# Optimization experiments

Hardware: AMD Instinct MI355X
Metric: run time of the kernel (lower is better)

The kernel has to match this reference:

```python
import jax, jax.numpy as jnp
import numpy as np

B, N, C, H = 16, 4096, 256, 4
D = C // H


def setup_inputs() -> dict:
    key = jax.random.key(0)
    ks = jax.random.split(key, 16)
    s = 0.02
    inp = {
        "x": jax.random.normal(ks[0], (B, N, C), jnp.float32),
        "encoding": jax.random.normal(ks[1], (2, B, 1, N, D), jnp.float32),
        "Wqkv_w": jax.random.normal(ks[2], (3 * C, C), jnp.float32) * s,
        "Wqkv_b": jnp.zeros((3 * C,), jnp.float32),
        "tssa_qkv_w": jax.random.normal(ks[3], (C, C), jnp.float32) * s,
        "tssa_qkv_b": jnp.zeros((C,), jnp.float32),
        "temp": jnp.ones((H, 1), jnp.float32),
        "tssa_out_w": jax.random.normal(ks[4], (C, C), jnp.float32) * s,
        "tssa_out_b": jnp.zeros((C,), jnp.float32),
        "out_proj_w": jax.random.normal(ks[5], (C, C), jnp.float32) * s,
        "out_proj_b": jnp.zeros((C,), jnp.float32),
        "ffn1_w": jax.random.normal(ks[6], (2 * C, 2 * C), jnp.float32) * s,
        "ffn1_b": jnp.zeros((2 * C,), jnp.float32),
        "ln_g": jnp.ones((2 * C,), jnp.float32),
        "ln_b": jnp.zeros((2 * C,), jnp.float32),
        "ffn2_w": jax.random.normal(ks[7], (C, 2 * C), jnp.float32) * s,
        "ffn2_b": jnp.zeros((C,), jnp.float32),
    }
    return inp


def _rotate_half(t):
    # (..., d) -> pairwise rotate: (x1, x2) -> (-x2, x1)
    t2 = t.reshape(t.shape[:-1] + (-1, 2))
    x1, x2 = t2[..., 0], t2[..., 1]
    return jnp.stack((-x2, x1), axis=-1).reshape(t.shape)


def reference(x, encoding, Wqkv_w, Wqkv_b, tssa_qkv_w, tssa_qkv_b, temp,
              tssa_out_w, tssa_out_b, out_proj_w, out_proj_b,
              ffn1_w, ffn1_b, ln_g, ln_b, ffn2_w, ffn2_b):
    b, n, c = x.shape
    h, d = H, D
    # QKV projection, layout (h, d, 3) on last dim as in unflatten(-1,(h,-1,3))
    qkv = (x @ Wqkv_w.T + Wqkv_b).reshape(b, n, h, d, 3).transpose(0, 2, 1, 3, 4)  # b h n d 3
    q, k, v = qkv[..., 0], qkv[..., 1], qkv[..., 2]
    rope = lambda t: t * encoding[0] + _rotate_half(t) * encoding[1]
    q = rope(q)
    k = rope(k)
    flat = lambda t: t.transpose(0, 2, 1, 3).reshape(b, n, c)  # b h n d -> b n (h d)
    w_input = (flat(q) + flat(k) + flat(v)) / 3.0
    # TSSA attention
    w = (w_input @ tssa_qkv_w.T + tssa_qkv_b).reshape(b, n, h, d).transpose(0, 2, 1, 3)  # b h n d
    norm = jnp.sqrt(jnp.sum(w * w, axis=2, keepdims=True))  # L2 over sequence axis N
    w_normed = w / jnp.maximum(norm, 1e-12)
    sum_ws = jnp.sum(w_normed * w_normed, axis=-1)  # b h n
    Pi = jax.nn.softmax(sum_ws * temp[None, :, :], axis=1)  # softmax over heads
    Pi_norm = Pi / (jnp.sum(Pi, axis=-1, keepdims=True) + 1e-8)
    dots = jnp.einsum('bhn,bhnd->bh', Pi_norm, w * w)  # (b,h,1,d) summed over d
    attn = 1.0 / (1.0 + dots)  # b h
    out = -(w * Pi[..., None]) * attn[:, :, None, None]  # b h n d
    out = out.transpose(0, 2, 1, 3).reshape(b, n, c)
    context = out @ tssa_out_w.T + tssa_out_b
    message = context @ out_proj_w.T + out_proj_b
    # residual FFN
    cat = jnp.concatenate([x, message], axis=-1)  # b n 2c
    h1 = cat @ ffn1_w.T + ffn1_b
    mu = jnp.mean(h1, axis=-1, keepdims=True)
    var = jnp.mean((h1 - mu) ** 2, axis=-1, keepdims=True)
    ln = (h1 - mu) / jnp.sqrt(var + 1e-5) * ln_g + ln_b
    g = jax.nn.gelu(ln, approximate=False)
    return x + (g @ ffn2_w.T + ffn2_b)
```

## Files before the change

kernel.cpp:

```cpp
#include <hip/hip_runtime.h>
#include <math.h>

#define Bc 16
#define Nc 4096

typedef __attribute__((ext_vector_type(8))) short short8;
typedef __attribute__((ext_vector_type(4))) float floatx4;

__device__ __forceinline__ unsigned short f2bf(float f) {
    union { float f; unsigned int u; } v; v.f = f;
    unsigned int u = v.u;
    return (unsigned short)((u + 0x7fffu + ((u >> 16) & 1u)) >> 16);
}
__device__ __forceinline__ float bf2f(unsigned short u) {
    union { unsigned int u; float f; } v; v.u = ((unsigned int)u) << 16;
    return v.f;
}

__device__ __forceinline__ float gelu_f(float x) {
    const float z = x * 0.70710678118654752f;
    const float az = fabsf(z);
    const float t = 1.f / (1.f + 0.3275911f * az);
    const float poly = t * (0.254829592f + t * (-0.284496736f +
                       t * (1.421413741f + t * (-1.453152027f + t * 1.061405429f))));
    const float e = __expf(-z * z);
    const float er = copysignf(1.f - poly * e, z);
    return 0.5f * x * (1.f + er);
}

__device__ __forceinline__ void gll16(const unsigned short* g, unsigned short* l) {
    __builtin_amdgcn_global_load_lds(
        (const __attribute__((address_space(1))) void*)g,
        (__attribute__((address_space(3))) void*)l,
        16, 0, 0);
}

template <int EPI, typename TOUT>
__global__ __launch_bounds__(512) void gemm_bf(
    const unsigned short* __restrict__ A0, int lda0,
    const unsigned short* __restrict__ A1, int lda1, int K0,
    const unsigned short* __restrict__ W,
    const float* __restrict__ bias,
    const unsigned short* __restrict__ resid_bf,
    const float* __restrict__ Pi,
    const float* __restrict__ Sb,
    const float* __restrict__ Tb,
    float* __restrict__ norm2,
    float* __restrict__ rowstats,
    const float* __restrict__ enc,
    const float* __restrict__ lng,
    const float* __restrict__ lnb,
    TOUT* __restrict__ C, int N, int K)
{
    __shared__ alignas(16) unsigned short As[128 * 64];
    __shared__ alignas(16) unsigned short Bs[256 * 64];

    const int t = threadIdx.x;
    const int bn = blockIdx.x, bm = blockIdx.y;
    const int lane = t & 63, wave = t >> 6;
    const int wm = wave >> 2, wn = wave & 3;
    const int quad = lane >> 4, l16 = lane & 15;
    const int rt = t >> 3, st = t & 7;

    float mean0 = 0.f, rstd0 = 0.f, mean1 = 0.f, rstd1 = 0.f;
    if constexpr (EPI == 3) {
        const size_t g0 = (size_t)bm * 128 + rt;
        const float2 s0 = *(const float2*)(rowstats + g0 * 2);
        const float2 s1 = *(const float2*)(rowstats + (g0 + 64) * 2);
        mean0 = s0.x * (1.f / 512.f);
        rstd0 = rsqrtf(s0.y * (1.f / 512.f) - mean0 * mean0 + 1e-5f);
        mean1 = s1.x * (1.f / 512.f);
        rstd1 = rsqrtf(s1.y * (1.f / 512.f) - mean1 * mean1 + 1e-5f);
    }

    floatx4 acc[4][4];
    #pragma unroll
    for (int i = 0; i < 4; ++i)
        #pragma unroll
        for (int j = 0; j < 4; ++j)
            acc[i][j] = (floatx4){0.f, 0.f, 0.f, 0.f};

    for (int k0 = 0; k0 < K; k0 += 64) {
        #pragma unroll
        for (int hh = 0; hh < 2; ++hh) {
            const int row = hh * 64 + rt;
            const int col = k0 + (st ^ (row & 7)) * 8;
            unsigned short* ldsa = As + row * 64 + st * 8;
            const size_t grow = (size_t)bm * 128 + row;
            if constexpr (EPI == 2) {
                const int b = (int)(grow >> 12);
                const int hd = col >> 6;
                const float Sv = Sb[b * 4 + hd], Tv = Tb[b * 4 + hd];
                const float at = 1.f / (1.f + Tv / (Sv + 1e-8f));
                const float sc = -Pi[grow * 4 + hd] * at;
                const short8 a = *(const short8*)(A0 + grow * (size_t)lda0 + col);
                short8 o;
                #pragma unroll
                for (int j = 0; j < 8; ++j) o[j] = (short)f2bf(bf2f((unsigned short)a[j]) * sc);
                *(short8*)ldsa = o;
            } else if constexpr (EPI == 3) {
                const float mean = hh ? mean1 : mean0;
                const float rstd = hh ? rstd1 : rstd0;
                const short8 a = *(const short8*)(A0 + grow * (size_t)lda0 + col);
                const float4 ga = *(const float4*)(lng + col);
                const float4 gb = *(const float4*)(lng + col + 4);
                const float4 ba = *(const float4*)(lnb + col);
                const float4 bb = *(const float4*)(lnb + col + 4);
                const float vg[8] = {ga.x, ga.y, ga.z, ga.w, gb.x, gb.y, gb.z, gb.w};
                const float vb[8] = {ba.x, ba.y, ba.z, ba.w, bb.x, bb.y, bb.z, bb.w};
                short8 o;
                #pragma unroll
                for (int jj = 0; jj < 8; ++jj) {
                    const float ln = (bf2f((unsigned short)a[jj]) - mean) * rstd * vg[jj] + vb[jj];
                    o[jj] = (short)f2bf(gelu_f(ln));
                }
                *(short8*)ldsa = o;
            } else {
                const unsigned short* src = (col < K0)
                    ? (A0 + grow * (size_t)lda0 + col)
                    : (A1 + grow * (size_t)lda1 + (col - K0));
                gll16(src, ldsa);
            }
        }
        #pragma unroll
        for (int hh = 0; hh < 4; ++hh) {
            const int row = hh * 64 + rt;
            const int col = k0 + (st ^ (row & 7)) * 8;
            gll16(W + ((size_t)bn * 256 + row) * (size_t)K + col, Bs + row * 64 + st * 8);
        }
        __syncthreads();
        #pragma unroll
        for (int kk = 0; kk < 2; ++kk) {
            short8 af[4], wf[4];
            #pragma unroll
            for (int i = 0; i < 4; ++i) {
                const int ra = wm * 64 + i * 16 + l16;
                af[i] = *(const short8*)(As + ra * 64 + ((quad + kk * 4) ^ (ra & 7)) * 8);
                const int rw = wn * 64 + i * 16 + l16;
                wf[i] = *(const short8*)(Bs + rw * 64 + ((quad + kk * 4) ^ (rw & 7)) * 8);
            }
            #pragma unroll
            for (int mi = 0; mi < 4; ++mi)
                #pragma unroll
                for (int ni = 0; ni < 4; ++ni)
                    acc[mi][ni] = __builtin_amdgcn_mfma_f32_16x16x32_bf16(
                        wf[ni], af[mi], acc[mi][ni], 0, 0, 0);
        }
        __syncthreads();
    }

    float rs[4], rq[4];
    if constexpr (EPI == 4) {
        #pragma unroll
        for (int m = 0; m < 4; ++m) { rs[m] = 0.f; rq[m] = 0.f; }
    }

    #pragma unroll
    for (int mi = 0; mi < 4; ++mi) {
        const size_t row = (size_t)bm * 128 + wm * 64 + mi * 16 + l16;
        #pragma unroll
        for (int ni = 0; ni < 4; ++ni) {
            const int cb = bn * 256 + wn * 64 + ni * 16 + quad * 4;
            const float4 b4 = *(const float4*)(bias + cb);
            if constexpr (EPI == 5) {
                const float s0 = acc[mi][ni][0] + b4.x;
                const float v0 = acc[mi][ni][1] + b4.y;
                const float s1 = acc[mi][ni][2] + b4.z;
                const float v1 = acc[mi][ni][3] + b4.w;
                const int j = cb >> 1;
                const int d = j & 63;
                const float2 e0 = *(const float2*)(enc + row * 64 + d);
                const float2 e1 = *(const float2*)(enc + 4194304 + row * 64 + d);
                const float r0 = s0 * e0.x - s1 * e1.x;
                const float r1 = s1 * e0.y + s0 * e1.y;
                ushort2 o;
                o.x = f2bf((r0 + v0) * (1.f / 3.f));
                o.y = f2bf((r1 + v1) * (1.f / 3.f));
                *(ushort2*)((unsigned short*)C + row * (size_t)N + j) = o;
            } else {
                float v[4] = {acc[mi][ni][0] + b4.x, acc[mi][ni][1] + b4.y,
                              acc[mi][ni][2] + b4.z, acc[mi][ni][3] + b4.w};
                if constexpr (EPI == 3) {
                    const ushort4 xr = *(const ushort4*)(resid_bf + row * (size_t)N + cb);
                    v[0] += bf2f(xr.x); v[1] += bf2f(xr.y);
                    v[2] += bf2f(xr.z); v[3] += bf2f(xr.w);
                }
                if constexpr (EPI == 4) {
                    #pragma unroll
                    for (int rg = 0; rg < 4; ++rg) { rs[mi] += v[rg]; rq[mi] += v[rg] * v[rg]; }
                }
                if constexpr (EPI == 1) {
                    float cs[4];
                    #pragma unroll
                    for (int rg = 0; rg < 4; ++rg) cs[rg] = v[rg] * v[rg];
                    #pragma unroll
                    for (int rg = 0; rg < 4; ++rg) {
                        float s = cs[rg];
                        s += __shfl_xor(s, 1, 64);
                        s += __shfl_xor(s, 2, 64);
                        s += __shfl_xor(s, 4, 64);
                        s += __shfl_xor(s, 8, 64);
                        if (l16 == 0) atomicAdd(&norm2[(bm >> 5) * 256 + cb + rg], s);
                    }
                }
                if constexpr (__is_same(TOUT, float)) {
                    float4 o; o.x = v[0]; o.y = v[1]; o.z = v[2]; o.w = v[3];
                    *(float4*)(C + row * (size_t)N + cb) = o;
                } else {
                    ushort4 o;
                    o.x = f2bf(v[0]); o.y = f2bf(v[1]); o.z = f2bf(v[2]); o.w = f2bf(v[3]);
                    *(ushort4*)(C + row * (size_t)N + cb) = o;
                }
            }
        }
    }
    if constexpr (EPI == 4) {
        #pragma unroll
        for (int mi = 0; mi < 4; ++mi) {
            float s = rs[mi], q = rq[mi];
            s += __shfl_xor(s, 16, 64); s += __shfl_xor(s, 32, 64);
            q += __shfl_xor(q, 16, 64); q += __shfl_xor(q, 32, 64);
            if (quad == 0) {
                const size_t row = (size_t)bm * 128 + wm * 64 + mi * 16 + l16;
                atomicAdd(&rowstats[row * 2], s);
                atomicAdd(&rowstats[row * 2 + 1], q);
            }
        }
    }
}

__device__ __forceinline__ void conv8(const float* src, unsigned short* dst, int i) {
    const float4 f0 = *(const float4*)(src + (size_t)i * 8);
    const float4 f1 = *(const float4*)(src + (size_t)i * 8 + 4);
    short8 sv;
    sv[0] = (short)f2bf(f0.x); sv[1] = (short)f2bf(f0.y);
    sv[2] = (short)f2bf(f0.z); sv[3] = (short)f2bf(f0.w);
    sv[4] = (short)f2bf(f1.x); sv[5] = (short)f2bf(f1.y);
    sv[6] = (short)f2bf(f1.z); sv[7] = (short)f2bf(f1.w);
    *(short8*)(dst + (size_t)i * 8) = sv;
}

__global__ __launch_bounds__(256) void prep_all(
    const float* __restrict__ x, const float* __restrict__ Wqkv,
    const float* __restrict__ bqkv, const float* __restrict__ tssa_w,
    const float* __restrict__ op_w, const float* __restrict__ to_w,
    const float* __restrict__ to_b, const float* __restrict__ op_b,
    const float* __restrict__ f1w, const float* __restrict__ f2w,
    unsigned short* __restrict__ x_bf, unsigned short* __restrict__ Wsv,
    float* __restrict__ bsv, unsigned short* __restrict__ tssa_bf,
    unsigned short* __restrict__ Wf, float* __restrict__ bfb,
    unsigned short* __restrict__ ffn1_bf, unsigned short* __restrict__ ffn2_bf,
    float* __restrict__ zbase, float* __restrict__ rowstats)
{
    const int blk = blockIdx.x, tt = threadIdx.x;
    if (blk < 8192) {
        conv8(x, x_bf, blk * 256 + tt);
    } else if (blk < 8704) {
        const int r = blk - 8192, c = tt;
        const int j = r >> 1;
        const int h = j >> 6, dd = j & 63;
        const int base = h * 192 + dd * 3;
        if (!(r & 1)) {
            Wsv[r * 256 + c] = f2bf(Wqkv[(base + 0) * 256 + c] + Wqkv[(base + 1) * 256 + c]);
            if (c == 0) bsv[r] = bqkv[base] + bqkv[base + 1];
        } else {
            Wsv[r * 256 + c] = f2bf(Wqkv[(base + 2) * 256 + c]);
            if (c == 0) bsv[r] = bqkv[base + 2];
        }
    } else if (blk < 8960) {
        const int i = blk - 8704;
        float s = 0.f;
        for (int k = 0; k < 256; ++k) s += op_w[i * 256 + k] * to_w[k * 256 + tt];
        Wf[i * 256 + tt] = f2bf(s);
    } else if (blk == 8960) {
        float s = op_b[tt];
        for (int k = 0; k < 256; ++k) s += op_w[tt * 256 + k] * to_b[k];
        bfb[tt] = s;
    } else if (blk < 8993) {
        conv8(tssa_w, tssa_bf, (blk - 8961) * 256 + tt);
    } else if (blk < 9121) {
        conv8(f1w, ffn1_bf, (blk - 8993) * 256 + tt);
    } else if (blk < 9185) {
        conv8(f2w, ffn2_bf, (blk - 9121) * 256 + tt);
    } else {
        const int i = (blk - 9185) * 256 + tt;
        if (i < 4288) zbase[i] = 0.f;
        else if (i < 135360) rowstats[i - 4288] = 0.f;
    }
}

__global__ __launch_bounds__(256) void pi_kernel(const unsigned short* __restrict__ w,
                                                 const float* __restrict__ norm2,
                                                 const float* __restrict__ temp,
                                                 float* __restrict__ Pi,
                                                 float* __restrict__ S,
                                                 float* __restrict__ T) {
    const int t = threadIdx.x;
    const int i = t & 15;
    const int lr = t >> 4;
    const size_t r = (size_t)blockIdx.x * 16 + lr;
    const int b = (int)(r >> 12);
    const unsigned short* wrow = w + r * 256;
    const float* n2row = norm2 + b * 256;
    float raw[4], nrm[4];
    #pragma unroll
    for (int h = 0; h < 4; ++h) {
        const ushort4 wv = *(const ushort4*)(wrow + h * 64 + i * 4);
        const float w0 = bf2f(wv.x), w1 = bf2f(wv.y), w2 = bf2f(wv.z), w3 = bf2f(wv.w);
        const float4 n2 = *(const float4*)(n2row + h * 64 + i * 4);
        const float s0 = w0 * w0, s1 = w1 * w1, s2 = w2 * w2, s3 = w3 * w3;
        raw[h] = s0 + s1 + s2 + s3;
        nrm[h] = s0 / fmaxf(n2.x, 1e-24f) + s1 / fmaxf(n2.y, 1e-24f)
               + s2 / fmaxf(n2.z, 1e-24f) + s3 / fmaxf(n2.w, 1e-24f);
    }
    #pragma unroll
    for (int off = 1; off < 16; off <<= 1) {
        #pragma unroll
        for (int h = 0; h < 4; ++h) {
            raw[h] += __shfl_xor(raw[h], off, 64);
            nrm[h] += __shfl_xor(nrm[h], off, 64);
        }
    }
    float sw[4], m = -1e30f;
    #pragma unroll
    for (int h = 0; h < 4; ++h) { sw[h] = nrm[h] * temp[h]; m = fmaxf(m, sw[h]); }
    float e[4], Z = 0.f;
    #pragma unroll
    for (int h = 0; h < 4; ++h) { e[h] = expf(sw[h] - m); Z += e[h]; }
    const float invZ = 1.f / Z;
    float pi[4];
    #pragma unroll
    for (int h = 0; h < 4; ++h) pi[h] = e[h] * invZ;
    if (i < 4) Pi[r * 4 + i] = pi[i];

    __shared__ float sS[16][4], sT[16][4];
    if (i == 0) {
        #pragma unroll
        for (int h = 0; h < 4; ++h) { sS[lr][h] = pi[h]; sT[lr][h] = pi[h] * raw[h]; }
    }
    __syncthreads();
    if (t < 4) {
        float as = 0.f, at = 0.f;
        for (int rr = 0; rr < 16; ++rr) { as += sS[rr][t]; at += sT[rr][t]; }
        atomicAdd(&S[b * 4 + t], as);
        atomicAdd(&T[b * 4 + t], at);
    }
}

extern "C" void kernel_launch(void* const* d_in, const int* in_sizes, int n_in,
                              void* d_out, int out_size, void* d_ws, size_t ws_size,
                              hipStream_t stream) {
    (void)in_sizes; (void)n_in; (void)out_size; (void)ws_size;
    const float* x          = (const float*)d_in[0];
    const float* enc        = (const float*)d_in[1];
    const float* Wqkv_w     = (const float*)d_in[2];
    const float* Wqkv_b     = (const float*)d_in[3];
    const float* tssa_qkv_w = (const float*)d_in[4];
    const float* tssa_qkv_b = (const float*)d_in[5];
    const float* temp       = (const float*)d_in[6];
    const float* tssa_out_w = (const float*)d_in[7];
    const float* tssa_out_b = (const float*)d_in[8];
    const float* out_proj_w = (const float*)d_in[9];
    const float* out_proj_b = (const float*)d_in[10];
    const float* ffn1_w     = (const float*)d_in[11];
    const float* ffn1_b     = (const float*)d_in[12];
    const float* ln_g       = (const float*)d_in[13];
    const float* ln_b       = (const float*)d_in[14];
    const float* ffn2_w     = (const float*)d_in[15];
    const float* ffn2_b     = (const float*)d_in[16];
    float* outp = (float*)d_out;

    const int M = Bc * Nc;

    char* ws = (char*)d_ws;
    unsigned short* x_bf  = (unsigned short*)(ws);
    unsigned short* wi_bf = (unsigned short*)(ws + (size_t)(32 << 20));
    unsigned short* h1_bf = (unsigned short*)(ws + (size_t)(32 << 20));
    unsigned short* w_bf  = (unsigned short*)(ws + (size_t)(64 << 20));
    unsigned short* msg_bf= (unsigned short*)(ws + (size_t)(96 << 20));
    float* fb    = (float*)(ws + (size_t)(128 << 20));
    float* Pi    = fb;
    float* norm2 = Pi + 262144;
    float* Sb    = norm2 + 4096;
    float* Tb    = Sb + 64;
    float* attnb = Tb + 64;
    float* bsv   = attnb + 64;
    float* bfb   = bsv + 512;
    float* rowstats = bfb + 256;
    unsigned short* Wsv_bf  = (unsigned short*)(rowstats + 131072);
    unsigned short* tssa_bf = Wsv_bf + 131072;
    unsigned short* Wf_bf   = tssa_bf + 65536;
    unsigned short* ffn1_bf = Wf_bf + 65536;
    unsigned short* ffn2_bf = ffn1_bf + 262144;

    prep_all<<<9714, 256, 0, stream>>>(
        x, Wqkv_w, Wqkv_b, tssa_qkv_w, out_proj_w, tssa_out_w, tssa_out_b,
        out_proj_b, ffn1_w, ffn2_w,
        x_bf, Wsv_bf, bsv, tssa_bf, Wf_bf, bfb, ffn1_bf, ffn2_bf,
        norm2, rowstats);

    gemm_bf<5, unsigned short><<<dim3(2, M / 128), 512, 0, stream>>>(
        x_bf, 256, x_bf, 256, 256, Wsv_bf, bsv,
        nullptr, nullptr, nullptr, nullptr, nullptr, nullptr,
        enc, nullptr, nullptr, wi_bf, 256, 256);

    gemm_bf<1, unsigned short><<<dim3(1, M / 128), 512, 0, stream>>>(
        wi_bf, 256, wi_bf, 256, 256, tssa_bf, tssa_qkv_b,
        nullptr, nullptr, nullptr, nullptr, norm2, nullptr,
        nullptr, nullptr, nullptr, w_bf, 256, 256);

    pi_kernel<<<4096, 256, 0, stream>>>(w_bf, norm2, temp, Pi, Sb, Tb);

    gemm_bf<2, unsigned short><<<dim3(1, M / 128), 512, 0, stream>>>(
        w_bf, 256, w_bf, 256, 256, Wf_bf, bfb,
        nullptr, Pi, Sb, Tb, nullptr, nullptr,
        nullptr, nullptr, nullptr, msg_bf, 256, 256);

    gemm_bf<4, unsigned short><<<dim3(2, M / 128), 512, 0, stream>>>(
        x_bf, 256, msg_bf, 256, 256, ffn1_bf, ffn1_b,
        nullptr, nullptr, nullptr, nullptr, nullptr, rowstats,
        nullptr, nullptr, nullptr, h1_bf, 512, 512);

    gemm_bf<3, float><<<dim3(1, M / 128), 512, 0, stream>>>(
        h1_bf, 512, h1_bf, 512, 512, ffn2_bf, ffn2_b,
        x_bf, nullptr, nullptr, nullptr, nullptr, rowstats,
        nullptr, ln_g, ln_b, outp, 256, 512);
}
```

Measured before the change: 465.4 us.

## Fold output projections into FFN1 weights and fuse message GEMM into FFN1

A new prep2 kernel multiplies the message half of the FFN1 weight by the combined tssa_out/out_proj weight, and folds the combined bias into a new FFN1 bias. The standalone message GEMM and its msg_bf intermediate are removed. The FFN1 GEMM now reads the scaled w activations directly for its second K half, applying the Pi/attention scaling while loading them. This saves one M×256×256 GEMM and a full write and read of the intermediate. The cost is an extra small weight-prep kernel on every call and extra rounding from folding the weights in bf16.

Result: slower. 482.4 us (+3.7%).

```diff
diff --git a/kernel.cpp b/kernel.cpp
--- a/kernel.cpp
+++ b/kernel.cpp
@@ -87,17 +87,21 @@
             const int col = k0 + (st ^ (row & 7)) * 8;
             unsigned short* ldsa = As + row * 64 + st * 8;
             const size_t grow = (size_t)bm * 128 + row;
-            if constexpr (EPI == 2) {
-                const int b = (int)(grow >> 12);
-                const int hd = col >> 6;
-                const float Sv = Sb[b * 4 + hd], Tv = Tb[b * 4 + hd];
-                const float at = 1.f / (1.f + Tv / (Sv + 1e-8f));
-                const float sc = -Pi[grow * 4 + hd] * at;
-                const short8 a = *(const short8*)(A0 + grow * (size_t)lda0 + col);
-                short8 o;
-                #pragma unroll
-                for (int j = 0; j < 8; ++j) o[j] = (short)f2bf(bf2f((unsigned short)a[j]) * sc);
-                *(short8*)ldsa = o;
+            if constexpr (EPI == 6) {
+                if (k0 < K0) {
+                    gll16(A0 + grow * (size_t)lda0 + col, ldsa);
+                } else {
+                    const int b = (int)(grow >> 12);
+                    const int hd = (col - K0) >> 6;
+                    const float Sv = Sb[b * 4 + hd], Tv = Tb[b * 4 + hd];
+                    const float at = 1.f / (1.f + Tv / (Sv + 1e-8f));
+                    const float sc = -Pi[grow * 4 + hd] * at;
+                    const short8 a = *(const short8*)(A1 + grow * (size_t)lda1 + (col - K0));
+                    short8 o;
+                    #pragma unroll
+                    for (int j = 0; j < 8; ++j) o[j] = (short)f2bf(bf2f((unsigned short)a[j]) * sc);
+                    *(short8*)ldsa = o;
+                }
             } else if constexpr (EPI == 3) {
                 const float mean = hh ? mean1 : mean0;
                 const float rstd = hh ? rstd1 : rstd0;
@@ -150,7 +154,7 @@
     }
 
     float rs[4], rq[4];
-    if constexpr (EPI == 4) {
+    if constexpr (EPI == 6) {
         #pragma unroll
         for (int m = 0; m < 4; ++m) { rs[m] = 0.f; rq[m] = 0.f; }
     }
@@ -185,7 +189,7 @@
                     v[0] += bf2f(xr.x); v[1] += bf2f(xr.y);
                     v[2] += bf2f(xr.z); v[3] += bf2f(xr.w);
                 }
-                if constexpr (EPI == 4) {
+                if constexpr (EPI == 6) {
                     #pragma unroll
                     for (int rg = 0; rg < 4; ++rg) { rs[mi] += v[rg]; rq[mi] += v[rg] * v[rg]; }
                 }
@@ -214,7 +218,7 @@
             }
         }
     }
-    if constexpr (EPI == 4) {
+    if constexpr (EPI == 6) {
         #pragma unroll
         for (int mi = 0; mi < 4; ++mi) {
             float s = rs[mi], q = rq[mi];
@@ -289,6 +293,26 @@
     }
 }
 
+__global__ __launch_bounds__(256) void prep2(
+    const float* __restrict__ f1w,
+    const float* __restrict__ f1b,
+    const unsigned short* __restrict__ Wf,
+    const float* __restrict__ bfb,
+    unsigned short* __restrict__ ffn1_bf,
+    float* __restrict__ cbias)
+{
+    const int j = blockIdx.x, k = threadIdx.x;
+    float s = 0.f;
+    for (int i = 0; i < 256; ++i)
+        s += f1w[(size_t)j * 512 + 256 + i] * bf2f(Wf[i * 256 + k]);
+    ffn1_bf[(size_t)j * 512 + 256 + k] = f2bf(s);
+    if (k == 0) {
+        float c = f1b[j];
+        for (int i = 0; i < 256; ++i) c += f1w[(size_t)j * 512 + 256 + i] * bfb[i];
+        cbias[j] = c;
+    }
+}
+
 __global__ __launch_bounds__(256) void pi_kernel(const unsigned short* __restrict__ w,
                                                  const float* __restrict__ norm2,
                                                  const float* __restrict__ temp,
@@ -377,14 +401,13 @@
     unsigned short* wi_bf = (unsigned short*)(ws + (size_t)(32 << 20));
     unsigned short* h1_bf = (unsigned short*)(ws + (size_t)(32 << 20));
     unsigned short* w_bf  = (unsigned short*)(ws + (size_t)(64 << 20));
-    unsigned short* msg_bf= (unsigned short*)(ws + (size_t)(96 << 20));
     float* fb    = (float*)(ws + (size_t)(128 << 20));
     float* Pi    = fb;
     float* norm2 = Pi + 262144;
     float* Sb    = norm2 + 4096;
     float* Tb    = Sb + 64;
-    float* attnb = Tb + 64;
-    float* bsv   = attnb + 64;
+    float* cbias = Tb + 64;
+    float* bsv   = cbias + 512;
     float* bfb   = bsv + 512;
     float* rowstats = bfb + 256;
     unsigned short* Wsv_bf  = (unsigned short*)(rowstats + 131072);
@@ -399,6 +422,8 @@
         x_bf, Wsv_bf, bsv, tssa_bf, Wf_bf, bfb, ffn1_bf, ffn2_bf,
         norm2, rowstats);
 
+    prep2<<<512, 256, 0, stream>>>(ffn1_w, ffn1_b, Wf_bf, bfb, ffn1_bf, cbias);
+
     gemm_bf<5, unsigned short><<<dim3(2, M / 128), 512, 0, stream>>>(
         x_bf, 256, x_bf, 256, 256, Wsv_bf, bsv,
         nullptr, nullptr, nullptr, nullptr, nullptr, nullptr,
@@ -411,14 +436,9 @@
 
     pi_kernel<<<4096, 256, 0, stream>>>(w_bf, norm2, temp, Pi, Sb, Tb);
 
-    gemm_bf<2, unsigned short><<<dim3(1, M / 128), 512, 0, stream>>>(
-        w_bf, 256, w_bf, 256, 256, Wf_bf, bfb,
-        nullptr, Pi, Sb, Tb, nullptr, nullptr,
-        nullptr, nullptr, nullptr, msg_bf, 256, 256);
-
-    gemm_bf<4, unsigned short><<<dim3(2, M / 128), 512, 0, stream>>>(
-        x_bf, 256, msg_bf, 256, 256, ffn1_bf, ffn1_b,
-        nullptr, nullptr, nullptr, nullptr, nullptr, rowstats,
+    gemm_bf<6, unsigned short><<<dim3(2, M / 128), 512, 0, stream>>>(
+        x_bf, 256, w_bf, 256, 256, ffn1_bf, cbias,
+        nullptr, Pi, Sb, Tb, nullptr, rowstats,
         nullptr, nullptr, nullptr, h1_bf, 512, 512);
 
     gemm_bf<3, float><<<dim3(1, M / 128), 512, 0, stream>>>(
```
